# Optimization experiments

Measured on AMD Instinct MI355X. Metric: run time of the kernel, lower is better.

Reference implementation:

```python
import jax, jax.numpy as jnp
import numpy as np

B, C, H, W = 16, 256, 64, 64
LDCE, CDCE = 100, 128


def _conv(x, w, groups=1):
    # x: NCHW, w: OIHW, stride 1, SAME padding (matches pad=1 for 3x3, pad=0 for 1x1)
    return jax.lax.conv_general_dilated(x, w, (1, 1), 'SAME',
                                        feature_group_count=groups,
                                        dimension_numbers=('NCHW', 'OIHW', 'NCHW'))


def _bn(x, g, b, eps=1e-5):
    # training-mode BatchNorm2d: biased batch stats over (N,H,W)
    m = jnp.mean(x, axis=(0, 2, 3), keepdims=True)
    v = jnp.var(x, axis=(0, 2, 3), keepdims=True)
    return g[None, :, None, None] * (x - m) * jax.lax.rsqrt(v + eps) + b[None, :, None, None]


def _silu(z):
    return z * jax.nn.sigmoid(z)


def setup_inputs() -> dict:
    key = jax.random.key(0)
    ks = jax.random.split(key, 18)
    f32 = jnp.float32
    s = 0.05
    d = {}
    d['x'] = jax.random.normal(ks[0], (B, C, H, W), f32)
    d['dce_output'] = jax.random.normal(ks[1], (B, LDCE, CDCE), f32)
    # DCE projection Linear(dce_dim -> out_feat)
    d['w_dce'] = jax.random.normal(ks[2], (C, CDCE), f32) * s
    d['b_dce'] = jax.random.normal(ks[3], (C,), f32) * s
    # per-channel 3x3 convs, stacked as a depthwise kernel (C,1,3,3)
    d['w_ch'] = jax.random.normal(ks[4], (C, 1, 3, 3), f32) * s
    # shrink / expand MLP
    d['w_shrink'] = jax.random.normal(ks[5], (C // 2, C), f32) * s
    d['b_shrink'] = jax.random.normal(ks[6], (C // 2,), f32) * s
    d['w_expand'] = jax.random.normal(ks[7], (C, C // 2), f32) * s
    d['b_expand'] = jax.random.normal(ks[8], (C,), f32) * s
    # ResBlock backbone: conv3x3 -> BN -> SiLU -> conv1x1 -> BN
    d['w_conv1'] = jax.random.normal(ks[9], (C, C, 3, 3), f32) * s
    d['g_bn1'] = jnp.ones((C,), f32)
    d['be_bn1'] = jnp.zeros((C,), f32)
    d['w_conv2'] = jax.random.normal(ks[10], (C, C, 1, 1), f32) * s
    d['g_bn2'] = jnp.ones((C,), f32)
    d['be_bn2'] = jnp.zeros((C,), f32)
    # shortcut: conv1x1 -> BN
    d['w_sc'] = jax.random.normal(ks[11], (C, C, 1, 1), f32) * s
    d['g_bns'] = jnp.ones((C,), f32)
    d['be_bns'] = jnp.zeros((C,), f32)
    return d


def reference(x, dce_output, w_dce, b_dce, w_ch, w_shrink, b_shrink,
              w_expand, b_expand, w_conv1, g_bn1, be_bn1, w_conv2, g_bn2,
              be_bn2, w_sc, g_bns, be_bns):
    C2 = w_dce.shape[0]
    # 1. AdaptiveAvgPool1d(1) over sequence, then Linear: (B, C2)
    dce_pooled = jnp.mean(dce_output, axis=1)            # (B, CDCE)
    dce_proj = dce_pooled @ w_dce.T + b_dce              # (B, C2)
    # 2. per-channel Conv2d(1,1,3) + global avg pool == depthwise conv + mean
    conv_out = _conv(x, w_ch, groups=C2)                 # (B, C2, H, W)
    spatial_proj = jnp.mean(conv_out, axis=(2, 3))       # (B, C2)
    # 3-5. modulation gate
    m = dce_proj * spatial_proj
    h = jax.nn.relu(m @ w_shrink.T + b_shrink)
    mod = jax.nn.sigmoid(h @ w_expand.T + b_expand)      # (B, C2)
    # 6. channel-wise modulation
    xm = x * mod[:, :, None, None]
    # 7. ResBlock
    bb = _silu(_bn(_conv(xm, w_conv1), g_bn1, be_bn1))
    bb = _bn(_conv(bb, w_conv2), g_bn2, be_bn2)
    sc = _bn(_conv(xm, w_sc), g_bns, be_bns)
    return _silu(bb + sc)
```

## Files before the change

kernel.cpp:

```cpp
#include <hip/hip_runtime.h>

typedef unsigned short u16;
typedef unsigned int   u32;
typedef __attribute__((ext_vector_type(8))) __bf16 bf16x8;
typedef __attribute__((ext_vector_type(4))) float  f32x4;

#define HW 4096
#define NPOS 65536
#define CH 256
#define MT 512
#define NMT 256
#define PIMG 4356

__device__ __forceinline__ u16 f2bf(float f){
  u32 u = __float_as_uint(f);
  u += 0x7FFFu + ((u >> 16) & 1u);
  return (u16)(u >> 16);
}
__device__ __forceinline__ float bflo(u32 p){ return __uint_as_float(p << 16); }
__device__ __forceinline__ float bfhi(u32 p){ return __uint_as_float(p & 0xFFFF0000u); }

#define GLL16(g, l) __builtin_amdgcn_global_load_lds( \
    (__attribute__((address_space(1))) void*)(g), \
    (__attribute__((address_space(3))) void*)(l), 16, 0, 0)

#define VM4() asm volatile("s_waitcnt vmcnt(4)" ::: "memory")
#define VM0() asm volatile("s_waitcnt vmcnt(0)" ::: "memory")
#define BAR() __builtin_amdgcn_s_barrier()
#define SP1() __builtin_amdgcn_s_setprio(1)
#define SP0() __builtin_amdgcn_s_setprio(0)

#define MMQ(Aa, Bb, IO, JO) \
  { _Pragma("unroll") for (int fi=0; fi<4; fi++){ \
      _Pragma("unroll") for (int fj=0; fj<2; fj++){ \
        acc[(IO)+fi][(JO)+fj] = __builtin_amdgcn_mfma_f32_16x16x32_bf16(Aa[0][fi], Bb[0][fj], acc[(IO)+fi][(JO)+fj], 0,0,0); \
        acc[(IO)+fi][(JO)+fj] = __builtin_amdgcn_mfma_f32_16x16x32_bf16(Aa[1][fi], Bb[1][fj], acc[(IO)+fi][(JO)+fj], 0,0,0); \
  } } }

#define RDA(dst, D, QOFF) \
  { _Pragma("unroll") for (int fi=0; fi<4; fi++){ \
      dst[0][fi] = *(const bf16x8*)&SH[(D) + aBase + (QOFF) + fi*1024 + kx0]; \
      dst[1][fi] = *(const bf16x8*)&SH[(D) + aBase + (QOFF) + fi*1024 + kx1]; \
  } }
#define RDB(dst, D, JOFF) \
  { _Pragma("unroll") for (int fj=0; fj<2; fj++){ \
      dst[0][fj] = *(const bf16x8*)&SH[(D) + bBase + (JOFF) + fj*1024 + kx0]; \
      dst[1][fj] = *(const bf16x8*)&SH[(D) + bBase + (JOFF) + fj*1024 + kx1]; \
  } }

__global__ __launch_bounds__(256) void k_statsx(const float* __restrict__ x, float* __restrict__ stats){
  int bc = blockIdx.x; int tid = threadIdx.x;
  const float* xp = x + (size_t)bc * HW;
  float S=0.f, r0=0.f, r1=0.f, c0=0.f, c1=0.f;
  #pragma unroll
  for (int k=0;k<4;k++){
    int i4 = tid + k*256;
    float4 v = ((const float4*)xp)[i4];
    int pos = i4*4; int h = pos>>6; int wb = pos&63;
    float sv = v.x+v.y+v.z+v.w;
    S += sv;
    if (h==0)  r0 += sv;
    if (h==63) r1 += sv;
    if (wb==0)  c0 += v.x;
    if (wb==60) c1 += v.w;
  }
  __shared__ float red[4][5];
  #pragma unroll
  for (int off=32; off>0; off>>=1){
    S  += __shfl_down(S, off);
    r0 += __shfl_down(r0, off);
    r1 += __shfl_down(r1, off);
    c0 += __shfl_down(c0, off);
    c1 += __shfl_down(c1, off);
  }
  if ((tid & 63) == 0){
    int w = tid >> 6;
    red[w][0]=S; red[w][1]=r0; red[w][2]=r1; red[w][3]=c0; red[w][4]=c1;
  }
  __syncthreads();
  if (tid == 0){
    float* o = stats + (size_t)bc * 9;
    for (int j=0;j<5;j++) o[j] = red[0][j]+red[1][j]+red[2][j]+red[3][j];
    o[5] = xp[0];
    o[6] = xp[63];
    o[7] = xp[4032];
    o[8] = xp[4095];
  }
}

__global__ __launch_bounds__(256) void k_gate(const float* __restrict__ dce,
    const float* __restrict__ stats, const float* __restrict__ wch,
    const float* __restrict__ w_dce, const float* __restrict__ b_dce,
    const float* __restrict__ w_sh, const float* __restrict__ b_sh,
    const float* __restrict__ w_ex, const float* __restrict__ b_ex,
    float* __restrict__ modb){
  int b = blockIdx.x, tid = threadIdx.x;
  __shared__ float pl[128];
  __shared__ float mbuf[256];
  __shared__ float hbuf[128];
  __shared__ float ptmp[256];
  {
    int k = tid & 127, half = tid >> 7;
    const float* p = dce + (size_t)b*12800 + half*50*128 + k;
    float s = 0.f;
    #pragma unroll 5
    for (int l=0;l<50;l++) s += p[l*128];
    ptmp[tid] = s;
  }
  __syncthreads();
  if (tid < 128) pl[tid] = (ptmp[tid] + ptmp[tid+128]) * 0.01f;
  __syncthreads();
  {
    int c = tid;
    const float* st = stats + (size_t)(b*256+c)*9;
    float S=st[0], r0=st[1], r1=st[2], cc0=st[3], cc1=st[4];
    float x00=st[5], x0W=st[6], xH0=st[7], xHW=st[8];
    float acc = 0.f;
    #pragma unroll
    for (int t=0;t<9;t++){
      int dh = t/3 - 1, dw = t%3 - 1;
      float R = (dh==1)? r0 : (dh==-1)? r1 : 0.f;
      float Cc = (dw==1)? cc0 : (dw==-1)? cc1 : 0.f;
      float X = 0.f;
      if (dh==1 && dw==1) X = x00;
      else if (dh==1 && dw==-1) X = x0W;
      else if (dh==-1 && dw==1) X = xH0;
      else if (dh==-1 && dw==-1) X = xHW;
      acc += wch[c*9+t] * (S - R - Cc + X);
    }
    float sp_ = acc * (1.f/4096.f);
    float dp = b_dce[c];
    const float4* wr = (const float4*)(w_dce + c*128);
    #pragma unroll 8
    for (int k4=0;k4<32;k4++){
      float4 w4 = wr[k4];
      dp += w4.x*pl[k4*4] + w4.y*pl[k4*4+1] + w4.z*pl[k4*4+2] + w4.w*pl[k4*4+3];
    }
    mbuf[c] = sp_ * dp;
  }
  __syncthreads();
  if (tid < 128){
    int j = tid;
    float acc = b_sh[j];
    const float4* wr = (const float4*)(w_sh + j*256);
    #pragma unroll 8
    for (int k4=0;k4<64;k4++){
      float4 w4 = wr[k4];
      acc += w4.x*mbuf[k4*4] + w4.y*mbuf[k4*4+1] + w4.z*mbuf[k4*4+2] + w4.w*mbuf[k4*4+3];
    }
    hbuf[j] = fmaxf(acc, 0.f);
  }
  __syncthreads();
  {
    int c = tid;
    float acc = b_ex[c];
    const float4* wr = (const float4*)(w_ex + c*128);
    #pragma unroll 8
    for (int k4=0;k4<32;k4++){
      float4 w4 = wr[k4];
      acc += w4.x*hbuf[k4*4] + w4.y*hbuf[k4*4+1] + w4.z*hbuf[k4*4+2] + w4.w*hbuf[k4*4+3];
    }
    modb[b*256+c] = 1.f/(1.f + __expf(-acc));
  }
}

__global__ __launch_bounds__(256) void k_wprep(const float* __restrict__ w1,
    const float* __restrict__ wsc, const float* __restrict__ w2,
    u16* __restrict__ w1t, u16* __restrict__ wsct, u16* __restrict__ w2t){
  int bx = blockIdx.x, ci = threadIdx.x;
  if (bx < 2304){
    int co = bx / 9, t = bx - co*9;
    w1t[(size_t)co*2304 + t*256 + ci] = f2bf(w1[(size_t)(co*256+ci)*9 + t]);
  } else if (bx < 2560){
    int i = (bx-2304)*256 + ci;
    wsct[i] = f2bf(wsc[i]);
  } else {
    int i = (bx-2560)*256 + ci;
    w2t[i] = f2bf(w2[i]);
  }
}

__global__ __launch_bounds__(256) void k_halo(u16* __restrict__ xm){
  int b = blockIdx.x, tid = threadIdx.x;
  uint4 zq = {0u,0u,0u,0u};
  for (int i = tid; i < 260; i += 256){
    int row, col;
    if (i < 66){ row = 0; col = i; }
    else if (i < 132){ row = 65; col = i - 66; }
    else { int j = i - 132; row = 1 + (j >> 1); col = (j & 1) * 65; }
    uint4* p = (uint4*)(xm + ((size_t)b*PIMG + row*66 + col)*256);
    #pragma unroll
    for (int q=0;q<32;q++) p[q] = zq;
  }
}

__global__ __launch_bounds__(256) void k_xm(const float* __restrict__ x, const float* __restrict__ modb,
                                            u16* __restrict__ xm){
  __shared__ __attribute__((aligned(16))) u16 tile[64*266];
  int pt = blockIdx.x, ct = blockIdx.y, tid = threadIdx.x;
  int b = pt >> 4;
  int rem = (pt & 15) << 8;
  int C0 = ct << 6;
  {
    int c = tid >> 2, q = tid & 3;
    const float* xp = x + ((size_t)(b*256 + C0 + c))*HW + rem;
    float mv = modb[b*256 + C0 + c];
    #pragma unroll
    for (int k=0;k<16;k++){
      int pos = q*64 + k*4;
      float4 v = *(const float4*)(xp + pos);
      u32 w0 = (u32)f2bf(v.x*mv) | ((u32)f2bf(v.y*mv) << 16);
      u32 w1 = (u32)f2bf(v.z*mv) | ((u32)f2bf(v.w*mv) << 16);
      u32* dst = (u32*)&tile[c*266 + pos];
      dst[0] = w0; dst[1] = w1;
    }
  }
  __syncthreads();
  {
    int g = tid & 7, p0 = tid >> 3;
    #pragma unroll
    for (int k=0;k<8;k++){
      int pos = p0 + k*32;
      u32 v0 = tile[(g*8+0)*266 + pos], v1 = tile[(g*8+1)*266 + pos];
      u32 v2 = tile[(g*8+2)*266 + pos], v3 = tile[(g*8+3)*266 + pos];
      u32 v4 = tile[(g*8+4)*266 + pos], v5 = tile[(g*8+5)*266 + pos];
      u32 v6 = tile[(g*8+6)*266 + pos], v7 = tile[(g*8+7)*266 + pos];
      uint4 pk;
      pk.x = v0 | (v1<<16); pk.y = v2 | (v3<<16);
      pk.z = v4 | (v5<<16); pk.w = v6 | (v7<<16);
      int gp = rem + pos;
      int h = gp >> 6, w = gp & 63;
      *(uint4*)(xm + ((size_t)b*PIMG + (h+1)*66 + (w+1))*256 + C0 + g*8) = pk;
    }
  }
}

template<int NTAPS, int APAD>
__global__ __launch_bounds__(512, 2) void k_gemm8p(const u16* __restrict__ A,
    const u16* __restrict__ Bw, u16* __restrict__ y,
    float* __restrict__ psum, float* __restrict__ psq){
  constexpr int KTOT = NTAPS*256;
  constexpr int NT = KTOT/64;
  constexpr int NI = NT/2;
  __shared__ __attribute__((aligned(16))) u16 SH[65536];
  int tid = threadIdx.x;
  int lane = tid & 63, wave = tid >> 6;
  int wm = wave >> 2, wn = wave & 3;
  int l15 = lane & 15, quad = lane >> 4;
  int bx = blockIdx.x;
  int mt = ((bx & 7) << 5) | (bx >> 3);
  int P0 = mt*256;

  int s3  = l15 & 7;
  int kx0 = ((quad)     ^ s3) * 8;
  int kx1 = ((4 | quad) ^ s3) * 8;
  int aBase = wm*8192 + l15*64;
  int bBase = 32768 + (wn>>1)*8192 + (wn&1)*4096 + l15*64;

  int r0  = tid >> 3;
  int csrc = ((tid & 7) ^ (r0 & 7)) * 8;

  auto pvoff = [&](int pos)->int{
    if constexpr (APAD){
      int b_ = pos >> 12, rm = pos & 4095;
      return (b_*PIMG + ((rm>>6)+1)*66 + (rm&63)+1)*256 + csrc;
    } else {
      return pos*256 + csrc;
    }
  };
  const int vA00 = pvoff(P0 + r0),        vA01 = pvoff(P0 + 64 + r0);
  const int vA10 = pvoff(P0 + 128 + r0),  vA11 = pvoff(P0 + 192 + r0);
  const int vB00 = (r0)*KTOT + csrc,       vB01 = (64 + r0)*KTOT + csrc;
  const int vB10 = (128 + r0)*KTOT + csrc, vB11 = (192 + r0)*KTOT + csrc;

  f32x4 acc[8][4];
  f32x4 zz = {0.f,0.f,0.f,0.f};
  #pragma unroll
  for (int i=0;i<8;i++)
    #pragma unroll
    for (int j=0;j<4;j++) acc[i][j] = zz;

  auto stageA = [&](int t, int ah){
    int base = (t&1)*16384 + ah*8192;
    int uoff;
    if constexpr (NTAPS == 9){
      int tap = t >> 2, t3 = (tap*11) >> 5;
      uoff = (tap + 63*t3 - 67)*256 + (t&3)*64;
    } else {
      uoff = t*64;
    }
    GLL16(A + uoff + (ah ? vA10 : vA00), SH + base + tid*8);
    GLL16(A + uoff + (ah ? vA11 : vA01), SH + base + 4096 + tid*8);
  };
  auto stageB = [&](int t, int bh){
    int base = 32768 + (t&1)*16384 + bh*8192;
    int uoff = t*64;
    GLL16(Bw + uoff + (bh ? vB10 : vB00), SH + base + tid*8);
    GLL16(Bw + uoff + (bh ? vB11 : vB01), SH + base + 4096 + tid*8);
  };

  stageA(0,0); stageA(0,1); stageB(0,0); stageB(0,1);
  stageA(1,0); stageA(1,1);
  VM4();
  BAR();

  bf16x8 aLo[2][4], aHi[2][4], bLo[2][2], bHi[2][2];

  for (int n=0; n<NI; ++n){
    const int t1 = 2*n+1;
    const bool pre = (n+1 < NI);
    RDA(aLo, 0, 0); RDB(bLo, 0, 0);
    stageB(t1, 0);
    BAR();
    SP1(); MMQ(aLo, bLo, 0, 0); SP0();
    BAR();
    RDA(aHi, 0, 4096);
    stageB(t1, 1);
    BAR();
    SP1(); MMQ(aHi, bLo, 4, 0); SP0();
    BAR();
    RDB(bHi, 0, 2048);
    if (pre) stageA(t1+1, 0);
    BAR();
    SP1(); MMQ(aHi, bHi, 4, 2); SP0();
    BAR();
    if (pre){ stageA(t1+1, 1); VM4(); } else { VM0(); }
    BAR();
    SP1(); MMQ(aLo, bHi, 0, 2); SP0();
    BAR();
    RDA(aLo, 16384, 0); RDB(bLo, 16384, 0);
    if (pre) stageB(t1+1, 0);
    BAR();
    SP1(); MMQ(aLo, bLo, 0, 0); SP0();
    BAR();
    RDA(aHi, 16384, 4096);
    if (pre) stageB(t1+1, 1);
    BAR();
    SP1(); MMQ(aHi, bLo, 4, 0); SP0();
    BAR();
    RDB(bHi, 16384, 2048);
    if (pre) stageA(t1+2, 0);
    BAR();
    SP1(); MMQ(aHi, bHi, 4, 2); SP0();
    BAR();
    if (pre){ stageA(t1+2, 1); VM4(); }
    BAR();
    SP1(); MMQ(aLo, bHi, 0, 2); SP0();
    BAR();
  }

  #pragma unroll
  for (int i=0;i<8;i++){
    int m = wm*128 + i*16 + quad*4;
    #pragma unroll
    for (int j=0;j<4;j++){
      int n = wn*64 + j*16 + l15;
      size_t base = ((size_t)(P0 + m))*CH + n;
      #pragma unroll
      for (int r=0;r<4;r++)
        y[base + (size_t)r*CH] = f2bf(acc[i][j][r]);
    }
  }
  float* SHf = (float*)SH;
  #pragma unroll
  for (int j=0;j<4;j++){
    float a=0.f, b=0.f;
    #pragma unroll
    for (int i=0;i<8;i++)
      #pragma unroll
      for (int r=0;r<4;r++){ float v = acc[i][j][r]; a += v; b += v*v; }
    a += __shfl_xor(a,16); b += __shfl_xor(b,16);
    a += __shfl_xor(a,32); b += __shfl_xor(b,32);
    if (quad==0){
      int idx = ((wave*4 + j)*16 + l15)*2;
      SHf[idx] = a; SHf[idx+1] = b;
    }
  }
  __syncthreads();
  if (tid < 256){
    int n = tid; int wnn = n>>6; int j = (n>>4)&3; int li = n&15;
    int i0 = (((wnn)*4 + j)*16 + li)*2;
    int i1 = (((4+wnn)*4 + j)*16 + li)*2;
    psum[(size_t)n*NMT + mt] = SHf[i0] + SHf[i1];
    psq [(size_t)n*NMT + mt] = SHf[i0+1] + SHf[i1+1];
  }
}

__global__ __launch_bounds__(64) void k_bnstat(const float* __restrict__ psum, const float* __restrict__ psq,
    const float* __restrict__ g, const float* __restrict__ be,
    float* __restrict__ scale, float* __restrict__ shift){
  int c = blockIdx.x, t = threadIdx.x;
  const float* ps = psum + (size_t)c*NMT;
  const float* pq = psq  + (size_t)c*NMT;
  float s=0.f, q=0.f;
  #pragma unroll
  for (int i=0;i<4;i++){ s += ps[t + i*64]; q += pq[t + i*64]; }
  #pragma unroll
  for (int off=32; off>0; off>>=1){
    s += __shfl_down(s, off);
    q += __shfl_down(q, off);
  }
  if (t == 0){
    float mean = s * (1.f/65536.f);
    float var  = q * (1.f/65536.f) - mean*mean;
    float rstd = rsqrtf(var + 1e-5f);
    float sc = g[c]*rstd;
    scale[c] = sc;
    shift[c] = be[c] - mean*sc;
  }
}

__global__ __launch_bounds__(256) void k_bb(const u16* __restrict__ y1, const float* __restrict__ sc1,
    const float* __restrict__ sh1, u16* __restrict__ bb){
  __shared__ float sc[256], sh[256];
  int tid = threadIdx.x;
  sc[tid] = sc1[tid]; sh[tid] = sh1[tid];
  __syncthreads();
  size_t i = ((size_t)blockIdx.x*256 + tid)*8;
  int c0 = (int)(i & 255);
  uint4 v = *(const uint4*)(y1 + i);
  u32 a[4] = {v.x, v.y, v.z, v.w};
  u32 o[4];
  #pragma unroll
  for (int p=0;p<4;p++){
    float zl = sc[c0+2*p]*bflo(a[p]) + sh[c0+2*p];
    float zh = sc[c0+2*p+1]*bfhi(a[p]) + sh[c0+2*p+1];
    float ol = zl/(1.f+__expf(-zl));
    float oh = zh/(1.f+__expf(-zh));
    o[p] = (u32)f2bf(ol) | ((u32)f2bf(oh) << 16);
  }
  uint4 w; w.x=o[0]; w.y=o[1]; w.z=o[2]; w.w=o[3];
  *(uint4*)(bb + i) = w;
}

__global__ __launch_bounds__(256) void k_final(const u16* __restrict__ y2, const u16* __restrict__ ysc,
    const float* __restrict__ sc2, const float* __restrict__ sh2,
    const float* __restrict__ scs, const float* __restrict__ shs,
    float* __restrict__ out){
  __shared__ __attribute__((aligned(16))) float tile[64*257];
  __shared__ float l2s[64], l2h[64], lss[64], lsh[64];
  int pt = blockIdx.x, ct = blockIdx.y, tid = threadIdx.x;
  int C0 = ct << 6;
  if (tid < 64){ l2s[tid]=sc2[C0+tid]; l2h[tid]=sh2[C0+tid]; lss[tid]=scs[C0+tid]; lsh[tid]=shs[C0+tid]; }
  __syncthreads();
  size_t P0 = (size_t)pt * 256;
  int b = pt >> 4; int rem = (pt & 15) << 8;
  {
    int g = tid & 7, p0 = tid >> 3;
    for (int k=0;k<8;k++){
      int pos = p0 + k*32;
      size_t off = (P0+pos)*CH + C0 + g*8;
      uint4 va = *(const uint4*)(y2 + off);
      uint4 vb = *(const uint4*)(ysc + off);
      u32 aa[4] = {va.x,va.y,va.z,va.w};
      u32 bv[4] = {vb.x,vb.y,vb.z,vb.w};
      #pragma unroll
      for (int p=0;p<4;p++){
        int c = g*8 + 2*p;
        float z0 = l2s[c]*bflo(aa[p]) + l2h[c] + lss[c]*bflo(bv[p]) + lsh[c];
        float z1 = l2s[c+1]*bfhi(aa[p]) + l2h[c+1] + lss[c+1]*bfhi(bv[p]) + lsh[c+1];
        tile[c*257 + pos]     = z0/(1.f+__expf(-z0));
        tile[(c+1)*257 + pos] = z1/(1.f+__expf(-z1));
      }
    }
  }
  __syncthreads();
  {
    int c = tid >> 2, q = tid & 3;
    float* op = out + ((size_t)(b*256 + C0 + c))*HW + rem;
    #pragma unroll
    for (int k=0;k<16;k++){
      int pos = q*64 + k*4;
      float4 v;
      v.x = tile[c*257 + pos];
      v.y = tile[c*257 + pos + 1];
      v.z = tile[c*257 + pos + 2];
      v.w = tile[c*257 + pos + 3];
      *(float4*)(op + pos) = v;
    }
  }
}

extern "C" void kernel_launch(void* const* d_in, const int* in_sizes, int n_in,
                              void* d_out, int out_size, void* d_ws, size_t ws_size,
                              hipStream_t stream){
  const float* x     = (const float*)d_in[0];
  const float* dce   = (const float*)d_in[1];
  const float* w_dce = (const float*)d_in[2];
  const float* b_dce = (const float*)d_in[3];
  const float* w_ch  = (const float*)d_in[4];
  const float* w_sh  = (const float*)d_in[5];
  const float* b_sh  = (const float*)d_in[6];
  const float* w_ex  = (const float*)d_in[7];
  const float* b_ex  = (const float*)d_in[8];
  const float* w_c1  = (const float*)d_in[9];
  const float* g1    = (const float*)d_in[10];
  const float* be1   = (const float*)d_in[11];
  const float* w_c2  = (const float*)d_in[12];
  const float* g2    = (const float*)d_in[13];
  const float* be2   = (const float*)d_in[14];
  const float* w_s   = (const float*)d_in[15];
  const float* gs    = (const float*)d_in[16];
  const float* bes   = (const float*)d_in[17];
  float* out = (float*)d_out;
  char* ws = (char*)d_ws;

  const size_t NB  = (size_t)NPOS*CH*2;
  const size_t XMB = (size_t)16*PIMG*CH*2;
  u16* xm  = (u16*)(ws);
  u16* y1  = (u16*)(ws + XMB);
  u16* ysc = (u16*)(ws + XMB + NB);
  u16* bb  = (u16*)(ws + XMB + 2*NB);
  char* p = ws + XMB + 3*NB;
  u16* w1t   = (u16*)p; p += (size_t)256*2304*2;
  u16* wsct  = (u16*)p; p += (size_t)256*256*2;
  u16* w2t   = (u16*)p; p += (size_t)256*256*2;
  float* statsx = (float*)p; p += (size_t)16*256*9*4;
  float* modb   = (float*)p; p += (size_t)16*256*4;
  float* p1s = (float*)p; p += (size_t)MT*256*4;
  float* p1q = (float*)p; p += (size_t)MT*256*4;
  float* pss = (float*)p; p += (size_t)MT*256*4;
  float* psqv= (float*)p; p += (size_t)MT*256*4;
  float* p2s = (float*)p; p += (size_t)MT*256*4;
  float* p2q = (float*)p; p += (size_t)MT*256*4;
  float* bn1sc = (float*)p; p += 1024;
  float* bn1sh = (float*)p; p += 1024;
  float* bnssc = (float*)p; p += 1024;
  float* bnssh = (float*)p; p += 1024;
  float* bn2sc = (float*)p; p += 1024;
  float* bn2sh = (float*)p; p += 1024;

  k_halo<<<16, 256, 0, stream>>>(xm);
  k_statsx<<<4096, 256, 0, stream>>>(x, statsx);
  k_wprep<<<2816, 256, 0, stream>>>(w_c1, w_s, w_c2, w1t, wsct, w2t);
  k_gate<<<16, 256, 0, stream>>>(dce, statsx, w_ch, w_dce, b_dce, w_sh, b_sh, w_ex, b_ex, modb);
  k_xm<<<dim3(256,4), 256, 0, stream>>>(x, modb, xm);
  k_gemm8p<9,1><<<256, 512, 0, stream>>>(xm, w1t, y1, p1s, p1q);
  k_bnstat<<<256, 64, 0, stream>>>(p1s, p1q, g1, be1, bn1sc, bn1sh);
  k_bb<<<8192, 256, 0, stream>>>(y1, bn1sc, bn1sh, bb);
  k_gemm8p<1,1><<<256, 512, 0, stream>>>(xm, wsct, ysc, pss, psqv);
  k_bnstat<<<256, 64, 0, stream>>>(pss, psqv, gs, bes, bnssc, bnssh);
  k_gemm8p<1,0><<<256, 512, 0, stream>>>(bb, w2t, y1 , p2s, p2q);
  k_bnstat<<<256, 64, 0, stream>>>(p2s, p2q, g2, be2, bn2sc, bn2sh);
  k_final<<<dim3(256,4), 256, 0, stream>>>(y1, ysc, bn2sc, bn2sh, bnssc, bnssh, out);
}
```

Baseline: 379.1 us.

## Restructure GEMM main loop schedule to overlap LDS reads with MFMA and halve barriers

Reorders the bf16 conv-GEMM main loop so LDS fragment reads for the next quarter-step are issued before the current MFMA block, instead of behind separate barriers. This cuts the barrier count per half-iteration roughly in half and adds sched_barrier fences so the compiler keeps the intended ordering. The vmcnt waits are retuned (VM2/VM6) to match the new issue order of global-to-LDS loads. Reading LDS buffers while async stages are in flight carries a risk of races if the wait counts are off, and an extra __syncthreads is added before the epilogue reuses shared memory.

Result: slower. 460.9 us (+21.6%).

```diff
diff --git a/kernel.cpp b/kernel.cpp
--- a/kernel.cpp
+++ b/kernel.cpp
@@ -24,9 +24,11 @@
     (__attribute__((address_space(1))) void*)(g), \
     (__attribute__((address_space(3))) void*)(l), 16, 0, 0)
 
+#define VM0() asm volatile("s_waitcnt vmcnt(0)" ::: "memory")
+#define VM2() asm volatile("s_waitcnt vmcnt(2)" ::: "memory")
 #define VM4() asm volatile("s_waitcnt vmcnt(4)" ::: "memory")
-#define VM0() asm volatile("s_waitcnt vmcnt(0)" ::: "memory")
-#define BAR() __builtin_amdgcn_s_barrier()
+#define VM6() asm volatile("s_waitcnt vmcnt(6)" ::: "memory")
+#define BARX() do { __builtin_amdgcn_s_barrier(); __builtin_amdgcn_sched_barrier(0); } while(0)
 #define SP1() __builtin_amdgcn_s_setprio(1)
 #define SP0() __builtin_amdgcn_s_setprio(0)
 
@@ -302,51 +304,51 @@
   stageA(0,0); stageA(0,1); stageB(0,0); stageB(0,1);
   stageA(1,0); stageA(1,1);
   VM4();
-  BAR();
+  BARX();
 
   bf16x8 aLo[2][4], aHi[2][4], bLo[2][2], bHi[2][2];
+  RDA(aLo, 0, 0); RDB(bLo, 0, 0);
 
   for (int n=0; n<NI; ++n){
     const int t1 = 2*n+1;
     const bool pre = (n+1 < NI);
-    RDA(aLo, 0, 0); RDB(bLo, 0, 0);
+    BARX();
+    RDA(aHi, 0, 4096);
     stageB(t1, 0);
-    BAR();
     SP1(); MMQ(aLo, bLo, 0, 0); SP0();
-    BAR();
-    RDA(aHi, 0, 4096);
+    BARX();
+    RDB(bHi, 0, 2048);
     stageB(t1, 1);
-    BAR();
     SP1(); MMQ(aHi, bLo, 4, 0); SP0();
-    BAR();
-    RDB(bHi, 0, 2048);
+    BARX();
     if (pre) stageA(t1+1, 0);
-    BAR();
     SP1(); MMQ(aHi, bHi, 4, 2); SP0();
-    BAR();
-    if (pre){ stageA(t1+1, 1); VM4(); } else { VM0(); }
-    BAR();
+    if (pre){ VM4(); } else { VM2(); }
+    BARX();
+    RDA(aHi, 16384, 4096);
+    RDB(bLo, 16384, 0);
+    if (pre) stageA(t1+1, 1);
     SP1(); MMQ(aLo, bHi, 0, 2); SP0();
-    BAR();
-    RDA(aLo, 16384, 0); RDB(bLo, 16384, 0);
+    BARX();
+    RDA(aLo, 16384, 0);
     if (pre) stageB(t1+1, 0);
-    BAR();
+    SP1(); MMQ(aHi, bLo, 4, 0); SP0();
+    if (pre){ VM6(); } else { VM0(); }
+    BARX();
+    RDB(bHi, 16384, 2048);
+    if (pre) stageB(t1+1, 1);
     SP1(); MMQ(aLo, bLo, 0, 0); SP0();
-    BAR();
-    RDA(aHi, 16384, 4096);
-    if (pre) stageB(t1+1, 1);
-    BAR();
-    SP1(); MMQ(aHi, bLo, 4, 0); SP0();
-    BAR();
-    RDB(bHi, 16384, 2048);
+    BARX();
     if (pre) stageA(t1+2, 0);
-    BAR();
+    SP1(); MMQ(aLo, bHi, 0, 2); SP0();
+    if (pre){ VM4(); }
+    BARX();
+    if (pre){
+      RDA(aLo, 0, 0);
+      RDB(bLo, 0, 0);
+      stageA(t1+2, 1);
+    }
     SP1(); MMQ(aHi, bHi, 4, 2); SP0();
-    BAR();
-    if (pre){ stageA(t1+2, 1); VM4(); }
-    BAR();
-    SP1(); MMQ(aLo, bHi, 0, 2); SP0();
-    BAR();
   }
 
   #pragma unroll
@@ -362,6 +364,7 @@
     }
   }
   float* SHf = (float*)SH;
+  __syncthreads();
   #pragma unroll
   for (int j=0;j<4;j++){
     float a=0.f, b=0.f;
```

## Fold channel modulation into per-batch weights and fuse stats into transpose pass

Applied to the files above, without the earlier changes.

The per-channel sigmoid gate is no longer applied to activations. It is folded into the conv1 and shortcut weights, producing per-batch bf16 weight copies, and the GEMMs offset the weight pointer by batch index. The separate x statistics pass is merged into the transpose/bf16-conversion kernel, which emits per-chunk partial sums that the gate kernel reduces. This drops one full read of x and splits the x→bf16 conversion from the gate dependency. In exchange the weight-prep kernel grows 16x, writing about 19MB of per-batch weights, and the GEMMs lose cross-batch weight cache reuse.

Result: slower. 393.7 us (+3.9%).

```diff
diff --git a/kernel.cpp b/kernel.cpp
--- a/kernel.cpp
+++ b/kernel.cpp
@@ -48,139 +48,7 @@
       dst[1][fj] = *(const bf16x8*)&SH[(D) + bBase + (JOFF) + fj*1024 + kx1]; \
   } }
 
-__global__ __launch_bounds__(256) void k_statsx(const float* __restrict__ x, float* __restrict__ stats){
-  int bc = blockIdx.x; int tid = threadIdx.x;
-  const float* xp = x + (size_t)bc * HW;
-  float S=0.f, r0=0.f, r1=0.f, c0=0.f, c1=0.f;
-  #pragma unroll
-  for (int k=0;k<4;k++){
-    int i4 = tid + k*256;
-    float4 v = ((const float4*)xp)[i4];
-    int pos = i4*4; int h = pos>>6; int wb = pos&63;
-    float sv = v.x+v.y+v.z+v.w;
-    S += sv;
-    if (h==0)  r0 += sv;
-    if (h==63) r1 += sv;
-    if (wb==0)  c0 += v.x;
-    if (wb==60) c1 += v.w;
-  }
-  __shared__ float red[4][5];
-  #pragma unroll
-  for (int off=32; off>0; off>>=1){
-    S  += __shfl_down(S, off);
-    r0 += __shfl_down(r0, off);
-    r1 += __shfl_down(r1, off);
-    c0 += __shfl_down(c0, off);
-    c1 += __shfl_down(c1, off);
-  }
-  if ((tid & 63) == 0){
-    int w = tid >> 6;
-    red[w][0]=S; red[w][1]=r0; red[w][2]=r1; red[w][3]=c0; red[w][4]=c1;
-  }
-  __syncthreads();
-  if (tid == 0){
-    float* o = stats + (size_t)bc * 9;
-    for (int j=0;j<5;j++) o[j] = red[0][j]+red[1][j]+red[2][j]+red[3][j];
-    o[5] = xp[0];
-    o[6] = xp[63];
-    o[7] = xp[4032];
-    o[8] = xp[4095];
-  }
-}
-
-__global__ __launch_bounds__(256) void k_gate(const float* __restrict__ dce,
-    const float* __restrict__ stats, const float* __restrict__ wch,
-    const float* __restrict__ w_dce, const float* __restrict__ b_dce,
-    const float* __restrict__ w_sh, const float* __restrict__ b_sh,
-    const float* __restrict__ w_ex, const float* __restrict__ b_ex,
-    float* __restrict__ modb){
-  int b = blockIdx.x, tid = threadIdx.x;
-  __shared__ float pl[128];
-  __shared__ float mbuf[256];
-  __shared__ float hbuf[128];
-  __shared__ float ptmp[256];
-  {
-    int k = tid & 127, half = tid >> 7;
-    const float* p = dce + (size_t)b*12800 + half*50*128 + k;
-    float s = 0.f;
-    #pragma unroll 5
-    for (int l=0;l<50;l++) s += p[l*128];
-    ptmp[tid] = s;
-  }
-  __syncthreads();
-  if (tid < 128) pl[tid] = (ptmp[tid] + ptmp[tid+128]) * 0.01f;
-  __syncthreads();
-  {
-    int c = tid;
-    const float* st = stats + (size_t)(b*256+c)*9;
-    float S=st[0], r0=st[1], r1=st[2], cc0=st[3], cc1=st[4];
-    float x00=st[5], x0W=st[6], xH0=st[7], xHW=st[8];
-    float acc = 0.f;
-    #pragma unroll
-    for (int t=0;t<9;t++){
-      int dh = t/3 - 1, dw = t%3 - 1;
-      float R = (dh==1)? r0 : (dh==-1)? r1 : 0.f;
-      float Cc = (dw==1)? cc0 : (dw==-1)? cc1 : 0.f;
-      float X = 0.f;
-      if (dh==1 && dw==1) X = x00;
-      else if (dh==1 && dw==-1) X = x0W;
-      else if (dh==-1 && dw==1) X = xH0;
-      else if (dh==-1 && dw==-1) X = xHW;
-      acc += wch[c*9+t] * (S - R - Cc + X);
-    }
-    float sp_ = acc * (1.f/4096.f);
-    float dp = b_dce[c];
-    const float4* wr = (const float4*)(w_dce + c*128);
-    #pragma unroll 8
-    for (int k4=0;k4<32;k4++){
-      float4 w4 = wr[k4];
-      dp += w4.x*pl[k4*4] + w4.y*pl[k4*4+1] + w4.z*pl[k4*4+2] + w4.w*pl[k4*4+3];
-    }
-    mbuf[c] = sp_ * dp;
-  }
-  __syncthreads();
-  if (tid < 128){
-    int j = tid;
-    float acc = b_sh[j];
-    const float4* wr = (const float4*)(w_sh + j*256);
-    #pragma unroll 8
-    for (int k4=0;k4<64;k4++){
-      float4 w4 = wr[k4];
-      acc += w4.x*mbuf[k4*4] + w4.y*mbuf[k4*4+1] + w4.z*mbuf[k4*4+2] + w4.w*mbuf[k4*4+3];
-    }
-    hbuf[j] = fmaxf(acc, 0.f);
-  }
-  __syncthreads();
-  {
-    int c = tid;
-    float acc = b_ex[c];
-    const float4* wr = (const float4*)(w_ex + c*128);
-    #pragma unroll 8
-    for (int k4=0;k4<32;k4++){
-      float4 w4 = wr[k4];
-      acc += w4.x*hbuf[k4*4] + w4.y*hbuf[k4*4+1] + w4.z*hbuf[k4*4+2] + w4.w*hbuf[k4*4+3];
-    }
-    modb[b*256+c] = 1.f/(1.f + __expf(-acc));
-  }
-}
-
-__global__ __launch_bounds__(256) void k_wprep(const float* __restrict__ w1,
-    const float* __restrict__ wsc, const float* __restrict__ w2,
-    u16* __restrict__ w1t, u16* __restrict__ wsct, u16* __restrict__ w2t){
-  int bx = blockIdx.x, ci = threadIdx.x;
-  if (bx < 2304){
-    int co = bx / 9, t = bx - co*9;
-    w1t[(size_t)co*2304 + t*256 + ci] = f2bf(w1[(size_t)(co*256+ci)*9 + t]);
-  } else if (bx < 2560){
-    int i = (bx-2304)*256 + ci;
-    wsct[i] = f2bf(wsc[i]);
-  } else {
-    int i = (bx-2560)*256 + ci;
-    w2t[i] = f2bf(w2[i]);
-  }
-}
-
-__global__ __launch_bounds__(256) void k_halo(u16* __restrict__ xm){
+__global__ __launch_bounds__(256) void k_halo(u16* __restrict__ xpad){
   int b = blockIdx.x, tid = threadIdx.x;
   uint4 zq = {0u,0u,0u,0u};
   for (int i = tid; i < 260; i += 256){
@@ -188,31 +56,53 @@
     if (i < 66){ row = 0; col = i; }
     else if (i < 132){ row = 65; col = i - 66; }
     else { int j = i - 132; row = 1 + (j >> 1); col = (j & 1) * 65; }
-    uint4* p = (uint4*)(xm + ((size_t)b*PIMG + row*66 + col)*256);
+    uint4* p = (uint4*)(xpad + ((size_t)b*PIMG + row*66 + col)*256);
     #pragma unroll
     for (int q=0;q<32;q++) p[q] = zq;
   }
 }
 
-__global__ __launch_bounds__(256) void k_xm(const float* __restrict__ x, const float* __restrict__ modb,
-                                            u16* __restrict__ xm){
+__global__ __launch_bounds__(256) void k_xt(const float* __restrict__ x,
+    u16* __restrict__ xpad, float* __restrict__ statsp, float* __restrict__ statsc){
   __shared__ __attribute__((aligned(16))) u16 tile[64*266];
   int pt = blockIdx.x, ct = blockIdx.y, tid = threadIdx.x;
   int b = pt >> 4;
-  int rem = (pt & 15) << 8;
+  int chunk = pt & 15;
+  int rem = chunk << 8;
   int C0 = ct << 6;
   {
     int c = tid >> 2, q = tid & 3;
     const float* xp = x + ((size_t)(b*256 + C0 + c))*HW + rem;
-    float mv = modb[b*256 + C0 + c];
+    float S = 0.f, c0t = 0.f, c1t = 0.f;
     #pragma unroll
     for (int k=0;k<16;k++){
       int pos = q*64 + k*4;
       float4 v = *(const float4*)(xp + pos);
-      u32 w0 = (u32)f2bf(v.x*mv) | ((u32)f2bf(v.y*mv) << 16);
-      u32 w1 = (u32)f2bf(v.z*mv) | ((u32)f2bf(v.w*mv) << 16);
+      S += v.x+v.y+v.z+v.w;
+      if (k==0)  c0t = v.x;
+      if (k==15) c1t = v.w;
+      u32 w0 = (u32)f2bf(v.x) | ((u32)f2bf(v.y) << 16);
+      u32 w1 = (u32)f2bf(v.z) | ((u32)f2bf(v.w) << 16);
       u32* dst = (u32*)&tile[c*266 + pos];
       dst[0] = w0; dst[1] = w1;
+    }
+    float Sown = S;
+    float S3  = __shfl_down(Sown, 3);
+    float c03 = __shfl_down(c0t, 3);
+    float c13 = __shfl_down(c1t, 3);
+    float S4 = S;  S4 += __shfl_down(S4, 1);  S4 += __shfl_down(S4, 2);
+    float c0s = c0t; c0s += __shfl_down(c0s, 1); c0s += __shfl_down(c0s, 2);
+    float c1s = c1t; c1s += __shfl_down(c1s, 1); c1s += __shfl_down(c1s, 2);
+    if (q == 0){
+      size_t plane = (size_t)(b*256 + C0 + c);
+      float* o = statsp + (plane*16 + chunk)*5;
+      o[0] = S4;
+      o[1] = (chunk==0)  ? Sown : 0.f;
+      o[2] = (chunk==15) ? S3   : 0.f;
+      o[3] = c0s;
+      o[4] = c1s;
+      if (chunk==0){  statsc[plane*4+0] = c0t; statsc[plane*4+1] = c1t; }
+      if (chunk==15){ statsc[plane*4+2] = c03; statsc[plane*4+3] = c13; }
     }
   }
   __syncthreads();
@@ -230,12 +120,115 @@
       pk.z = v4 | (v5<<16); pk.w = v6 | (v7<<16);
       int gp = rem + pos;
       int h = gp >> 6, w = gp & 63;
-      *(uint4*)(xm + ((size_t)b*PIMG + (h+1)*66 + (w+1))*256 + C0 + g*8) = pk;
-    }
-  }
-}
-
-template<int NTAPS, int APAD>
+      *(uint4*)(xpad + ((size_t)b*PIMG + (h+1)*66 + (w+1))*256 + C0 + g*8) = pk;
+    }
+  }
+}
+
+__global__ __launch_bounds__(256) void k_gate(const float* __restrict__ dce,
+    const float* __restrict__ statsp, const float* __restrict__ statsc,
+    const float* __restrict__ wch,
+    const float* __restrict__ w_dce, const float* __restrict__ b_dce,
+    const float* __restrict__ w_sh, const float* __restrict__ b_sh,
+    const float* __restrict__ w_ex, const float* __restrict__ b_ex,
+    float* __restrict__ modb){
+  int b = blockIdx.x, tid = threadIdx.x;
+  __shared__ float pl[128];
+  __shared__ float mbuf[256];
+  __shared__ float hbuf[128];
+  __shared__ float ptmp[256];
+  {
+    int k = tid & 127, half = tid >> 7;
+    const float* p = dce + (size_t)b*12800 + half*50*128 + k;
+    float s = 0.f;
+    #pragma unroll 5
+    for (int l=0;l<50;l++) s += p[l*128];
+    ptmp[tid] = s;
+  }
+  __syncthreads();
+  if (tid < 128) pl[tid] = (ptmp[tid] + ptmp[tid+128]) * 0.01f;
+  __syncthreads();
+  {
+    int c = tid;
+    size_t plane = (size_t)(b*256 + c);
+    float s5[5] = {0.f,0.f,0.f,0.f,0.f};
+    const float* pp = statsp + plane*80;
+    #pragma unroll
+    for (int ch=0; ch<16; ch++)
+      #pragma unroll
+      for (int j=0;j<5;j++) s5[j] += pp[ch*5 + j];
+    float S=s5[0], r0=s5[1], r1=s5[2], cc0=s5[3], cc1=s5[4];
+    const float* cn = statsc + plane*4;
+    float x00=cn[0], x0W=cn[1], xH0=cn[2], xHW=cn[3];
+    float acc = 0.f;
+    #pragma unroll
+    for (int t=0;t<9;t++){
+      int dh = t/3 - 1, dw = t%3 - 1;
+      float R = (dh==1)? r0 : (dh==-1)? r1 : 0.f;
+      float Cc = (dw==1)? cc0 : (dw==-1)? cc1 : 0.f;
+      float X = 0.f;
+      if (dh==1 && dw==1) X = x00;
+      else if (dh==1 && dw==-1) X = x0W;
+      else if (dh==-1 && dw==1) X = xH0;
+      else if (dh==-1 && dw==-1) X = xHW;
+      acc += wch[c*9+t] * (S - R - Cc + X);
+    }
+    float sp_ = acc * (1.f/4096.f);
+    float dp = b_dce[c];
+    const float4* wr = (const float4*)(w_dce + c*128);
+    #pragma unroll 8
+    for (int k4=0;k4<32;k4++){
+      float4 w4 = wr[k4];
+      dp += w4.x*pl[k4*4] + w4.y*pl[k4*4+1] + w4.z*pl[k4*4+2] + w4.w*pl[k4*4+3];
+    }
+    mbuf[c] = sp_ * dp;
+  }
+  __syncthreads();
+  if (tid < 128){
+    int j = tid;
+    float acc = b_sh[j];
+    const float4* wr = (const float4*)(w_sh + j*256);
+    #pragma unroll 8
+    for (int k4=0;k4<64;k4++){
+      float4 w4 = wr[k4];
+      acc += w4.x*mbuf[k4*4] + w4.y*mbuf[k4*4+1] + w4.z*mbuf[k4*4+2] + w4.w*mbuf[k4*4+3];
+    }
+    hbuf[j] = fmaxf(acc, 0.f);
+  }
+  __syncthreads();
+  {
+    int c = tid;
+    float acc = b_ex[c];
+    const float4* wr = (const float4*)(w_ex + c*128);
+    #pragma unroll 8
+    for (int k4=0;k4<32;k4++){
+      float4 w4 = wr[k4];
+      acc += w4.x*hbuf[k4*4] + w4.y*hbuf[k4*4+1] + w4.z*hbuf[k4*4+2] + w4.w*hbuf[k4*4+3];
+    }
+    modb[b*256+c] = 1.f/(1.f + __expf(-acc));
+  }
+}
+
+__global__ __launch_bounds__(256) void k_wfold(const float* __restrict__ w1,
+    const float* __restrict__ wsc, const float* __restrict__ w2,
+    const float* __restrict__ modb,
+    u16* __restrict__ w1b, u16* __restrict__ wscb, u16* __restrict__ w2t){
+  int bx = blockIdx.x, ci = threadIdx.x;
+  if (bx < 36864){
+    int b = bx / 2304; int rest = bx - b*2304;
+    int o = rest / 9, t = rest - o*9;
+    w1b[(size_t)(b*256+o)*2304 + t*256 + ci] =
+        f2bf(w1[(size_t)(o*256+ci)*9 + t] * modb[b*256+ci]);
+  } else if (bx < 36864+4096){
+    int i = bx - 36864; int b = i >> 8, o = i & 255;
+    wscb[(size_t)(b*256+o)*256 + ci] = f2bf(wsc[o*256+ci] * modb[b*256+ci]);
+  } else {
+    int o = bx - (36864+4096);
+    w2t[o*256 + ci] = f2bf(w2[o*256+ci]);
+  }
+}
+
+template<int NTAPS, int APAD, int BSTR>
 __global__ __launch_bounds__(512, 2) void k_gemm8p(const u16* __restrict__ A,
     const u16* __restrict__ Bw, u16* __restrict__ y,
     float* __restrict__ psum, float* __restrict__ psq){
@@ -250,6 +243,7 @@
   int bx = blockIdx.x;
   int mt = ((bx & 7) << 5) | (bx >> 3);
   int P0 = mt*256;
+  if constexpr (BSTR) Bw += (size_t)(mt >> 4) * BSTR;
 
   int s3  = l15 & 7;
   int kx0 = ((quad)     ^ s3) * 8;
@@ -507,15 +501,16 @@
 
   const size_t NB  = (size_t)NPOS*CH*2;
   const size_t XMB = (size_t)16*PIMG*CH*2;
-  u16* xm  = (u16*)(ws);
-  u16* y1  = (u16*)(ws + XMB);
-  u16* ysc = (u16*)(ws + XMB + NB);
-  u16* bb  = (u16*)(ws + XMB + 2*NB);
+  u16* xpad = (u16*)(ws);
+  u16* y1   = (u16*)(ws + XMB);
+  u16* ysc  = (u16*)(ws + XMB + NB);
+  u16* bb   = (u16*)(ws + XMB + 2*NB);
   char* p = ws + XMB + 3*NB;
-  u16* w1t   = (u16*)p; p += (size_t)256*2304*2;
-  u16* wsct  = (u16*)p; p += (size_t)256*256*2;
+  u16* w1b   = (u16*)p; p += (size_t)16*256*2304*2;
+  u16* wscb  = (u16*)p; p += (size_t)16*256*256*2;
   u16* w2t   = (u16*)p; p += (size_t)256*256*2;
-  float* statsx = (float*)p; p += (size_t)16*256*9*4;
+  float* statsp = (float*)p; p += (size_t)4096*16*5*4;
+  float* statsc = (float*)p; p += (size_t)4096*4*4;
   float* modb   = (float*)p; p += (size_t)16*256*4;
   float* p1s = (float*)p; p += (size_t)MT*256*4;
   float* p1q = (float*)p; p += (size_t)MT*256*4;
@@ -530,17 +525,16 @@
   float* bn2sc = (float*)p; p += 1024;
   float* bn2sh = (float*)p; p += 1024;
 
-  k_halo<<<16, 256, 0, stream>>>(xm);
-  k_statsx<<<4096, 256, 0, stream>>>(x, statsx);
-  k_wprep<<<2816, 256, 0, stream>>>(w_c1, w_s, w_c2, w1t, wsct, w2t);
-  k_gate<<<16, 256, 0, stream>>>(dce, statsx, w_ch, w_dce, b_dce, w_sh, b_sh, w_ex, b_ex, modb);
-  k_xm<<<dim3(256,4), 256, 0, stream>>>(x, modb, xm);
-  k_gemm8p<9,1><<<256, 512, 0, stream>>>(xm, w1t, y1, p1s, p1q);
+  k_halo<<<16, 256, 0, stream>>>(xpad);
+  k_xt<<<dim3(256,4), 256, 0, stream>>>(x, xpad, statsp, statsc);
+  k_gate<<<16, 256, 0, stream>>>(dce, statsp, statsc, w_ch, w_dce, b_dce, w_sh, b_sh, w_ex, b_ex, modb);
+  k_wfold<<<36864+4096+256, 256, 0, stream>>>(w_c1, w_s, w_c2, modb, w1b, wscb, w2t);
+  k_gemm8p<9,1,589824><<<256, 512, 0, stream>>>(xpad, w1b, y1, p1s, p1q);
   k_bnstat<<<256, 64, 0, stream>>>(p1s, p1q, g1, be1, bn1sc, bn1sh);
   k_bb<<<8192, 256, 0, stream>>>(y1, bn1sc, bn1sh, bb);
-  k_gemm8p<1,1><<<256, 512, 0, stream>>>(xm, wsct, ysc, pss, psqv);
+  k_gemm8p<1,1,65536><<<256, 512, 0, stream>>>(xpad, wscb, ysc, pss, psqv);
   k_bnstat<<<256, 64, 0, stream>>>(pss, psqv, gs, bes, bnssc, bnssh);
-  k_gemm8p<1,0><<<256, 512, 0, stream>>>(bb, w2t, y1 , p2s, p2q);
+  k_gemm8p<1,0,0><<<256, 512, 0, stream>>>(bb, w2t, y1 , p2s, p2q);
   k_bnstat<<<256, 64, 0, stream>>>(p2s, p2q, g2, be2, bn2sc, bn2sh);
   k_final<<<dim3(256,4), 256, 0, stream>>>(y1, ysc, bn2sc, bn2sh, bnssc, bnssh, out);
 }
```
